# Optimization experiments

Hardware: AMD Instinct MI355X
Metric: run time of the kernel (lower is better)

Reference implementation:

```python
import jax, jax.numpy as jnp
import numpy as np

B, T, S, D, H = 16, 128, 128, 512, 100

def setup_inputs() -> dict:
    key = jax.random.key(0)
    ks = jax.random.split(key, 10)
    sc = 0.02
    return {
        "input": jax.random.normal(ks[0], (B, T, D), dtype=jnp.float32),
        "memory_bank": jax.random.normal(ks[1], (B, S, D), dtype=jnp.float32),
        "W_in": jax.random.normal(ks[2], (D, D), dtype=jnp.float32) * sc,   # linear_in, no bias
        "W1": jax.random.normal(ks[3], (H, 2 * D), dtype=jnp.float32) * sc,  # linear_1
        "b1": jnp.zeros((H,), dtype=jnp.float32),
        "W2": jax.random.normal(ks[4], (H, H), dtype=jnp.float32) * sc,      # linear_2
        "b2": jnp.zeros((H,), dtype=jnp.float32),
        "w_mean": jax.random.normal(ks[5], (H,), dtype=jnp.float32) * sc,    # mean_out
        "b_mean": jnp.zeros((1,), dtype=jnp.float32),
        "w_var": jax.random.normal(ks[6], (H,), dtype=jnp.float32) * sc,     # var_out
        "b_var": jnp.zeros((1,), dtype=jnp.float32),
        "W_out": jax.random.normal(ks[7], (D, 2 * D), dtype=jnp.float32) * sc,  # linear_out, no bias
    }


def reference(input, memory_bank, W_in, W1, b1, W2, b2, w_mean, b_mean, w_var, b_var, W_out):
    d = input.shape[-1]
    # score(): linear_in(h_t) then bmm with h_s^T -> [B,T,S]
    ht = jnp.einsum('btd,ed->bte', input, W_in)
    align = jnp.einsum('bte,bse->bts', ht, memory_bank)
    # softmax over source dim (no memory_lengths -> no mask)
    align_vectors = jax.nn.softmax(align, axis=-1)
    # get_raw_scores(): fused form of cat([h_t_expand, h_s_expand]) @ W1^T
    W1t, W1s = W1[:, :d], W1[:, d:]
    pt = jnp.einsum('btd,hd->bth', input, W1t)        # [B,T,H]
    ps = jnp.einsum('bsd,hd->bsh', memory_bank, W1s)  # [B,S,H]
    h1 = jax.nn.softplus(pt[:, :, None, :] + ps[:, None, :, :] + b1)  # [B,T,S,H]
    h2 = jax.nn.softplus(jnp.einsum('btsh,gh->btsg', h1, W2) + b2)    # [B,T,S,H]
    h_mean = jax.nn.softplus(jnp.einsum('btsg,g->bts', h2, w_mean) + b_mean[0])
    h_var = jax.nn.softplus(jnp.einsum('btsg,g->bts', h2, w_var) + b_var[0])
    # context + output projection + tanh
    c = jnp.einsum('bts,bsd->btd', align_vectors, memory_bank)
    concat_c = jnp.concatenate([c, input], axis=-1)  # [B,T,2D]
    attn_h = jnp.tanh(jnp.einsum('btf,df->btd', concat_c, W_out))
    # multi-step: transpose to [T,B,*]
    attn_h = jnp.transpose(attn_h, (1, 0, 2))
    align_vectors = jnp.transpose(align_vectors, (1, 0, 2))
    return attn_h, align_vectors, h_mean, h_var
```

## Files before the change

### kernel.cpp

```cpp
#include <hip/hip_runtime.h>
#include <hip/hip_bf16.h>
#include <math.h>

#define Bn 16
#define Tn 128
#define Sn 128
#define Dn 512
#define Hn 100
#define TT 4

typedef short short8 __attribute__((ext_vector_type(8)));
typedef float f32x4 __attribute__((ext_vector_type(4)));
typedef unsigned short ushort4v __attribute__((ext_vector_type(4)));

__device__ __forceinline__ float softplus_f(float x) {
    return fmaxf(x, 0.0f) + __logf(1.0f + __expf(-fabsf(x)));
}
__device__ __forceinline__ unsigned short f2bf(float f) {
    unsigned u = __float_as_uint(f);
    unsigned r = u + 0x7FFFu + ((u >> 16) & 1u);
    return (unsigned short)(r >> 16);
}
__device__ __forceinline__ float bf2f(unsigned short h) {
    return __uint_as_float(((unsigned)h) << 16);
}
__device__ __forceinline__ unsigned pkrn(float a, float b) {
    __hip_bfloat162 h = __float22bfloat162_rn(float2{a, b});
    return *reinterpret_cast<unsigned*>(&h);
}
struct BfPair { unsigned short h, l; };
__device__ __forceinline__ BfPair split2(float x) {
    BfPair p;
    p.h = f2bf(x);
    p.l = f2bf(x - bf2f(p.h));
    return p;
}

__global__ __launch_bounds__(256)
void conv_trans(const float* __restrict__ input, const float* __restrict__ mem,
                const float* __restrict__ W_in, const float* __restrict__ W1,
                const float* __restrict__ W_out, const float* __restrict__ W2,
                unsigned short* __restrict__ inh, unsigned short* __restrict__ inl,
                unsigned short* __restrict__ memh, unsigned short* __restrict__ meml,
                unsigned short* __restrict__ winh, unsigned short* __restrict__ winl,
                unsigned short* __restrict__ w1b, unsigned short* __restrict__ woutb,
                unsigned short* __restrict__ w2b, unsigned short* __restrict__ concatb,
                unsigned short* __restrict__ memTb)
{
    __shared__ float tile[64][65];
    const int bx = blockIdx.x;
    if (bx >= 2930) {
        const int b2x = bx - 2930;
        const int d0 = (b2x & 7) * 64, s0 = ((b2x >> 3) & 1) * 64, b = b2x >> 4;
        const int tid = threadIdx.x;
        const int r = tid >> 2, cb = (tid & 3) * 16;
        const float* src = mem + ((long)b * Sn + s0 + r) * Dn + d0 + cb;
        #pragma unroll
        for (int j = 0; j < 4; ++j) {
            float4 v = *(const float4*)&src[j * 4];
            tile[r][cb + j * 4 + 0] = v.x;
            tile[r][cb + j * 4 + 1] = v.y;
            tile[r][cb + j * 4 + 2] = v.z;
            tile[r][cb + j * 4 + 3] = v.w;
        }
        __syncthreads();
        unsigned short* dst = memTb + ((long)b * Dn + d0 + r) * Sn + s0 + cb;
        #pragma unroll
        for (int j = 0; j < 4; ++j) {
            ushort4v q;
            q.x = f2bf(tile[cb + j * 4 + 0][r]);
            q.y = f2bf(tile[cb + j * 4 + 1][r]);
            q.z = f2bf(tile[cb + j * 4 + 2][r]);
            q.w = f2bf(tile[cb + j * 4 + 3][r]);
            *(ushort4v*)&dst[j * 4] = q;
        }
        return;
    }
    long gid = (long)bx * 1024 + (long)threadIdx.x * 4;
    if (gid < 1048576) {
        float4 v = *(const float4*)&input[gid];
        BfPair a = split2(v.x), b = split2(v.y), c = split2(v.z), d = split2(v.w);
        ushort4v h = {a.h, b.h, c.h, d.h};
        ushort4v l = {a.l, b.l, c.l, d.l};
        *(ushort4v*)&inh[gid] = h;
        *(ushort4v*)&inl[gid] = l;
        long row = gid >> 9; int col = (int)(gid & 511);
        *(ushort4v*)&concatb[row * 1024 + 512 + col] = h;
    } else if (gid < 2097152) {
        long e = gid - 1048576;
        float4 v = *(const float4*)&mem[e];
        BfPair a = split2(v.x), b = split2(v.y), c = split2(v.z), d = split2(v.w);
        ushort4v h = {a.h, b.h, c.h, d.h};
        ushort4v l = {a.l, b.l, c.l, d.l};
        *(ushort4v*)&memh[e] = h;
        *(ushort4v*)&meml[e] = l;
    } else if (gid < 2359296) {
        long e = gid - 2097152;
        float4 v = *(const float4*)&W_in[e];
        BfPair a = split2(v.x), b = split2(v.y), c = split2(v.z), d = split2(v.w);
        ushort4v h = {a.h, b.h, c.h, d.h};
        ushort4v l = {a.l, b.l, c.l, d.l};
        *(ushort4v*)&winh[e] = h;
        *(ushort4v*)&winl[e] = l;
    } else if (gid < 2461696) {
        long e = gid - 2359296;
        float4 v = *(const float4*)&W1[e];
        ushort4v h = {f2bf(v.x), f2bf(v.y), f2bf(v.z), f2bf(v.w)};
        *(ushort4v*)&w1b[e] = h;
    } else if (gid < 2985984) {
        long e = gid - 2461696;
        float4 v = *(const float4*)&W_out[e];
        ushort4v h = {f2bf(v.x), f2bf(v.y), f2bf(v.z), f2bf(v.w)};
        *(ushort4v*)&woutb[e] = h;
    } else {
        long e = gid - 2985984;
        int n = (int)(e >> 7), k = (int)(e & 127);
        ushort4v h;
        #pragma unroll
        for (int j = 0; j < 4; ++j) {
            int kj = k + j;
            float val = (n < Hn && kj < Hn) ? W2[n * Hn + kj] : 0.0f;
            h[j] = f2bf(val);
        }
        *(ushort4v*)&w2b[n * 128 + k] = h;
    }
}

template<int SPLIT, int EPI, int KSPLIT, int BSEL>
__device__ __forceinline__
void gemm_body(int bx, int by, int bz_in, int upperThresh,
               const unsigned short* __restrict__ Ah, const unsigned short* __restrict__ Al,
               const unsigned short* __restrict__ Bh, const unsigned short* __restrict__ Bl,
               float* __restrict__ C, unsigned short* __restrict__ Cb,
               unsigned short* __restrict__ Cb2, const float* __restrict__ bias,
               int N, int K, int lda, int ldb, int ldc,
               long sA, long sB, long sC, long sKC,
               unsigned short* As_, unsigned short* Bs_)
{
    unsigned short* Asl = As_ + 4096;
    unsigned short* Bsl = Bs_ + 4096;

    const int tid = threadIdx.x;
    const int n0 = bx * 64;
    const long m0 = (long)by * 64;
    int bz = bz_in, kh = 0;
    if (KSPLIT) { bz = bz_in & 15; kh = bz_in >> 4; }
    Ah += (long)bz * sA;
    Bh += (long)bz * sB;
    if (SPLIT) { Al += (long)bz * sA; Bl += (long)bz * sB; }
    const bool upperB = BSEL && (by >= upperThresh);
    if (upperB) Bh += BSEL;

    const int kbeg = KSPLIT ? kh * (K / KSPLIT) : 0;
    const int kend = KSPLIT ? kbeg + (K / KSPLIT) : K;

    const int wid = tid >> 6, lane = tid & 63;
    const int lm = lane & 15, lq = lane >> 4;
    const int wm = wid & 1, wn = wid >> 1;

    const int sr = tid >> 2;
    const int sc = (tid & 3) * 2;
    const bool bok = (n0 + sr) < N;

    f32x4 acc[2][2];
    #pragma unroll
    for (int i = 0; i < 2; ++i)
        #pragma unroll
        for (int j = 0; j < 2; ++j)
            acc[i][j] = (f32x4){0.f, 0.f, 0.f, 0.f};

    for (int k0 = kbeg; k0 < kend; k0 += 64) {
        __syncthreads();
        #pragma unroll
        for (int i = 0; i < 2; ++i) {
            int c = sc + i, p = c ^ (sr & 7);
            *(short8*)&As_[sr * 64 + p * 8] =
                *(const short8*)&Ah[(m0 + sr) * lda + k0 + c * 8];
            if (SPLIT)
                *(short8*)&Asl[sr * 64 + p * 8] =
                    *(const short8*)&Al[(m0 + sr) * lda + k0 + c * 8];
        }
        #pragma unroll
        for (int i = 0; i < 2; ++i) {
            int c = sc + i, p = c ^ (sr & 7);
            short8 v = {0, 0, 0, 0, 0, 0, 0, 0};
            short8 vl = {0, 0, 0, 0, 0, 0, 0, 0};
            if (bok) {
                v = *(const short8*)&Bh[(long)(n0 + sr) * ldb + k0 + c * 8];
                if (SPLIT) vl = *(const short8*)&Bl[(long)(n0 + sr) * ldb + k0 + c * 8];
            }
            *(short8*)&Bs_[sr * 64 + p * 8] = v;
            if (SPLIT) *(short8*)&Bsl[sr * 64 + p * 8] = vl;
        }
        __syncthreads();
        #pragma unroll
        for (int kst = 0; kst < 2; ++kst) {
            short8 a[2], b[2], a2[2], b2r[2];
            const int pp = (kst * 4 + lq) ^ (lm & 7);
            #pragma unroll
            for (int mt = 0; mt < 2; ++mt) {
                int row = wm * 32 + mt * 16 + lm;
                a[mt] = *(const short8*)&As_[row * 64 + pp * 8];
                if (SPLIT) a2[mt] = *(const short8*)&Asl[row * 64 + pp * 8];
            }
            #pragma unroll
            for (int nt = 0; nt < 2; ++nt) {
                int row = wn * 32 + nt * 16 + lm;
                b[nt] = *(const short8*)&Bs_[row * 64 + pp * 8];
                if (SPLIT) b2r[nt] = *(const short8*)&Bsl[row * 64 + pp * 8];
            }
            #pragma unroll
            for (int mt = 0; mt < 2; ++mt)
                #pragma unroll
                for (int nt = 0; nt < 2; ++nt) {
                    if (SPLIT) {
                        acc[mt][nt] = __builtin_amdgcn_mfma_f32_16x16x32_bf16(
                            a2[mt], b[nt], acc[mt][nt], 0, 0, 0);
                        acc[mt][nt] = __builtin_amdgcn_mfma_f32_16x16x32_bf16(
                            a[mt], b2r[nt], acc[mt][nt], 0, 0, 0);
                    }
                    acc[mt][nt] = __builtin_amdgcn_mfma_f32_16x16x32_bf16(
                        a[mt], b[nt], acc[mt][nt], 0, 0, 0);
                }
        }
    }

    #pragma unroll
    for (int mt = 0; mt < 2; ++mt)
        #pragma unroll
        for (int nt = 0; nt < 2; ++nt)
            #pragma unroll
            for (int r = 0; r < 4; ++r) {
                long m = m0 + wm * 32 + mt * 16 + lq * 4 + r;
                int n = n0 + wn * 32 + nt * 16 + lm;
                float v = acc[mt][nt][r];
                if (EPI == 0) {
                    if (n < N)
                        C[(long)bz * sC + (long)kh * sKC + m * ldc + n] = v;
                } else if (EPI == 1) {
                    unsigned short h = f2bf(v);
                    Cb[m * ldc + n] = h;
                    Cb2[m * ldc + n] = f2bf(v - bf2f(h));
                } else if (EPI == 2) {
                    long bb = m >> 7, tt = m & 127;
                    C[tt * (Bn * Dn) + bb * Dn + n] = tanhf(v);
                } else if (EPI == 3) {
                    Cb[(long)bz * sC + m * ldc + n] = f2bf(v);
                } else {
                    float bb = (!upperB && n < Hn) ? bias[n] : 0.f;
                    C[m * ldc + n] = v + bb;
                }
            }
}

template<int SPLIT, int EPI, int KSPLIT, int BSEL>
__global__ __launch_bounds__(256)
void mfma_gemm3(const unsigned short* __restrict__ Ah, const unsigned short* __restrict__ Al,
                const unsigned short* __restrict__ Bh, const unsigned short* __restrict__ Bl,
                float* __restrict__ C, unsigned short* __restrict__ Cb,
                unsigned short* __restrict__ Cb2, const float* __restrict__ bias,
                int N, int K, int lda, int ldb, int ldc,
                long sA, long sB, long sC, long sKC)
{
    __shared__ __align__(16) unsigned short As_[(SPLIT ? 2 : 1) * 4096];
    __shared__ __align__(16) unsigned short Bs_[(SPLIT ? 2 : 1) * 4096];
    gemm_body<SPLIT, EPI, KSPLIT, BSEL>(blockIdx.x, blockIdx.y, blockIdx.z,
        (int)(gridDim.y >> 1), Ah, Al, Bh, Bl, C, Cb, Cb2, bias,
        N, K, lda, ldb, ldc, sA, sB, sC, sKC, As_, Bs_);
}

__global__ __launch_bounds__(256)
void gemm_ht_ptps(const unsigned short* __restrict__ inh, const unsigned short* __restrict__ inl,
                  const unsigned short* __restrict__ winh, const unsigned short* __restrict__ winl,
                  unsigned short* __restrict__ hth, unsigned short* __restrict__ htl,
                  const unsigned short* __restrict__ w1b, float* __restrict__ ptps,
                  const float* __restrict__ b1)
{
    __shared__ __align__(16) unsigned short As_[8192];
    __shared__ __align__(16) unsigned short Bs_[8192];
    const int id = blockIdx.x;
    if (id < 256) {
        gemm_body<1, 1, 0, 0>(id & 7, id >> 3, 0, 0,
            inh, inl, winh, winl, nullptr, hth, htl, nullptr,
            Dn, Dn, Dn, Dn, Dn, 0L, 0L, 0L, 0L, As_, Bs_);
    } else {
        const int j = id - 256;
        gemm_body<0, 4, 0, 512>(j & 1, j >> 1, 0, 32,
            inh, nullptr, w1b, nullptr, ptps, nullptr, nullptr, b1,
            Hn, Dn, Dn, 2 * Dn, 128, 0L, 0L, 0L, 0L, As_, Bs_);
    }
}

__global__ __launch_bounds__(256)
void mlp_mfma5(const float* __restrict__ ptps,
               const unsigned short* __restrict__ w2b,
               const float* __restrict__ b2,
               const float* __restrict__ w_mean, const float* __restrict__ b_mean,
               const float* __restrict__ w_var, const float* __restrict__ b_var,
               float* __restrict__ mean_out, float* __restrict__ var_out)
{
    __shared__ __align__(16) unsigned short w2s[112 * 128];
    __shared__ float ptl[TT][132];
    __shared__ float wpk[224];
    __shared__ float b2l[112];

    const int tg = blockIdx.x;
    const int b  = blockIdx.y & 15;
    const int s0 = (blockIdx.y >> 4) * 64;
    const int tid = threadIdx.x;

    #pragma unroll
    for (int i0 = 0; i0 < 7; ++i0) {
        int i = tid + i0 * 256;
        int r_ = i >> 4, c_ = i & 15;
        *(short8*)&w2s[r_ * 128 + (c_ ^ (r_ & 7)) * 8] = *(const short8*)&w2b[i * 8];
    }
    #pragma unroll
    for (int j = 0; j < 2; ++j) {
        int i = tid + j * 256;
        int tt = i >> 7, c = i & 127;
        ptl[tt][c] = ptps[((long)b * Tn + tg * TT + tt) * 128 + c];
    }
    if (tid < 224) {
        int g = tid >> 1;
        wpk[tid] = (g < Hn) ? ((tid & 1) ? w_var[g] : w_mean[g]) : 0.f;
    }
    if (tid < 112) b2l[tid] = (tid < Hn) ? b2[tid] : 0.f;

    const int wid = tid >> 6, lane = tid & 63;
    const int lm = lane & 15, lq = lane >> 4;
    const int s = s0 + wid * 16 + lm;

    float psreg[4][8];
    {
        const float* psrow = ptps + (long)(2048 + b * Sn + s) * 128;
        #pragma unroll
        for (int ks = 0; ks < 4; ++ks) {
            *(float4*)&psreg[ks][0] = *(const float4*)&psrow[ks * 32 + lq * 8];
            *(float4*)&psreg[ks][4] = *(const float4*)&psrow[ks * 32 + lq * 8 + 4];
        }
    }
    const float bm = b_mean[0], bv = b_var[0];
    __syncthreads();

    for (int t = 0; t < TT; ++t) {
        f32x4 acc[7];
        #pragma unroll
        for (int j = 0; j < 7; ++j) acc[j] = (f32x4){0.f, 0.f, 0.f, 0.f};

        #pragma unroll
        for (int ks = 0; ks < 4; ++ks) {
            float4 pa = *(const float4*)&ptl[t][ks * 32 + lq * 8];
            float4 pb = *(const float4*)&ptl[t][ks * 32 + lq * 8 + 4];
            float x0 = softplus_f(psreg[ks][0] + pa.x);
            float x1 = softplus_f(psreg[ks][1] + pa.y);
            float x2 = softplus_f(psreg[ks][2] + pa.z);
            float x3 = softplus_f(psreg[ks][3] + pa.w);
            float x4 = softplus_f(psreg[ks][4] + pb.x);
            float x5 = softplus_f(psreg[ks][5] + pb.y);
            float x6 = softplus_f(psreg[ks][6] + pb.z);
            float x7 = softplus_f(psreg[ks][7] + pb.w);
            union { uint4 u4; short8 s8; } cv;
            cv.u4.x = pkrn(x0, x1); cv.u4.y = pkrn(x2, x3);
            cv.u4.z = pkrn(x4, x5); cv.u4.w = pkrn(x6, x7);
            const short8 hf = cv.s8;
            const int p = (ks * 4 + lq) ^ (lm & 7);
            #pragma unroll
            for (int mt = 0; mt < 7; ++mt) {
                short8 w = *(const short8*)&w2s[(mt * 16 + lm) * 128 + p * 8];
                acc[mt] = __builtin_amdgcn_mfma_f32_16x16x32_bf16(w, hf, acc[mt], 0, 0, 0);
            }
        }
        float sM = 0.f, sV = 0.f;
        #pragma unroll
        for (int mt = 0; mt < 7; ++mt) {
            const int g0 = mt * 16 + lq * 4;
            float4 bg = *(const float4*)&b2l[g0];
            float4 wa = *(const float4*)&wpk[g0 * 2];
            float4 wb = *(const float4*)&wpk[g0 * 2 + 4];
            float h2;
            h2 = softplus_f(acc[mt][0] + bg.x); sM = fmaf(h2, wa.x, sM); sV = fmaf(h2, wa.y, sV);
            h2 = softplus_f(acc[mt][1] + bg.y); sM = fmaf(h2, wa.z, sM); sV = fmaf(h2, wa.w, sV);
            h2 = softplus_f(acc[mt][2] + bg.z); sM = fmaf(h2, wb.x, sM); sV = fmaf(h2, wb.y, sV);
            h2 = softplus_f(acc[mt][3] + bg.w); sM = fmaf(h2, wb.z, sM); sV = fmaf(h2, wb.w, sV);
        }
        sM += __shfl_xor(sM, 16); sM += __shfl_xor(sM, 32);
        sV += __shfl_xor(sV, 16); sV += __shfl_xor(sV, 32);
        if (lq == 0) {
            const long base = ((long)b * Tn + tg * TT + t) * Sn + s;
            mean_out[base] = softplus_f(sM + bm);
            var_out[base]  = softplus_f(sV + bv);
        }
    }
}

__global__ __launch_bounds__(256)
void softmax_c(const float* __restrict__ algn, long kstride,
               const unsigned short* __restrict__ memTb,
               float* __restrict__ av_out, unsigned short* __restrict__ concatb)
{
    __shared__ __align__(16) unsigned short avs[64 * 128];
    __shared__ __align__(16) unsigned short Bs[64 * 128];

    const int ntb = blockIdx.x, mtb = blockIdx.y, b = blockIdx.z;
    const int tid = threadIdx.x;
    const int r = tid >> 2, q = tid & 3;

    float v[32];
    {
        const float* arow = algn + ((long)b * Tn + mtb * 64 + r) * Sn + q * 32;
        #pragma unroll
        for (int j = 0; j < 8; ++j) {
            float4 a0 = *(const float4*)&arow[j * 4];
            float4 a1 = *(const float4*)&arow[j * 4 + kstride];
            float4 a2 = *(const float4*)&arow[j * 4 + 2 * kstride];
            float4 a3 = *(const float4*)&arow[j * 4 + 3 * kstride];
            v[j * 4 + 0] = a0.x + a1.x + a2.x + a3.x;
            v[j * 4 + 1] = a0.y + a1.y + a2.y + a3.y;
            v[j * 4 + 2] = a0.z + a1.z + a2.z + a3.z;
            v[j * 4 + 3] = a0.w + a1.w + a2.w + a3.w;
        }
    }
    float mx = v[0];
    #pragma unroll
    for (int i = 1; i < 32; ++i) mx = fmaxf(mx, v[i]);
    mx = fmaxf(mx, __shfl_xor(mx, 1));
    mx = fmaxf(mx, __shfl_xor(mx, 2));
    float sum = 0.f;
    #pragma unroll
    for (int i = 0; i < 32; ++i) { v[i] = __expf(v[i] - mx); sum += v[i]; }
    sum += __shfl_xor(sum, 1);
    sum += __shfl_xor(sum, 2);
    const float inv = 1.0f / sum;

    if (ntb == 0) {
        float* dst = av_out + (long)(mtb * 64 + r) * (Bn * Sn) + b * Sn + q * 32;
        #pragma unroll
        for (int j = 0; j < 8; ++j) {
            float4 o = {v[j*4]*inv, v[j*4+1]*inv, v[j*4+2]*inv, v[j*4+3]*inv};
            *(float4*)&dst[j * 4] = o;
        }
    }
    #pragma unroll
    for (int i = 0; i < 4; ++i) {
        int c = q * 4 + i;
        uint4 u;
        u.x = pkrn(v[i*8+0]*inv, v[i*8+1]*inv);
        u.y = pkrn(v[i*8+2]*inv, v[i*8+3]*inv);
        u.z = pkrn(v[i*8+4]*inv, v[i*8+5]*inv);
        u.w = pkrn(v[i*8+6]*inv, v[i*8+7]*inv);
        *(uint4*)&avs[r * 128 + (c ^ (r & 7)) * 8] = u;
    }
    #pragma unroll
    for (int j = 0; j < 4; ++j) {
        int idx = tid * 4 + j;
        int rB = idx >> 4, cB = idx & 15;
        *(short8*)&Bs[rB * 128 + (cB ^ (rB & 7)) * 8] =
            *(const short8*)&memTb[((long)b * Dn + ntb * 64 + rB) * Sn + cB * 8];
    }
    __syncthreads();

    const int wid = tid >> 6, lane = tid & 63;
    const int lm = lane & 15, lq = lane >> 4;
    const int wm = wid & 1, wn = wid >> 1;

    f32x4 acc[2][2];
    #pragma unroll
    for (int i = 0; i < 2; ++i)
        #pragma unroll
        for (int j = 0; j < 2; ++j) acc[i][j] = (f32x4){0.f, 0.f, 0.f, 0.f};

    #pragma unroll
    for (int kk = 0; kk < 4; ++kk) {
        const int p = (kk * 4 + lq) ^ (lm & 7);
        short8 a0 = *(const short8*)&avs[(wm * 32 + lm) * 128 + p * 8];
        short8 a1 = *(const short8*)&avs[(wm * 32 + 16 + lm) * 128 + p * 8];
        short8 b0 = *(const short8*)&Bs[(wn * 32 + lm) * 128 + p * 8];
        short8 b1 = *(const short8*)&Bs[(wn * 32 + 16 + lm) * 128 + p * 8];
        acc[0][0] = __builtin_amdgcn_mfma_f32_16x16x32_bf16(a0, b0, acc[0][0], 0, 0, 0);
        acc[0][1] = __builtin_amdgcn_mfma_f32_16x16x32_bf16(a0, b1, acc[0][1], 0, 0, 0);
        acc[1][0] = __builtin_amdgcn_mfma_f32_16x16x32_bf16(a1, b0, acc[1][0], 0, 0, 0);
        acc[1][1] = __builtin_amdgcn_mfma_f32_16x16x32_bf16(a1, b1, acc[1][1], 0, 0, 0);
    }
    #pragma unroll
    for (int mt = 0; mt < 2; ++mt)
        #pragma unroll
        for (int nt = 0; nt < 2; ++nt)
            #pragma unroll
            for (int rr = 0; rr < 4; ++rr) {
                long mrow = (long)b * Tn + mtb * 64 + wm * 32 + mt * 16 + lq * 4 + rr;
                int n = ntb * 64 + wn * 32 + nt * 16 + lm;
                concatb[mrow * 1024 + n] = f2bf(acc[mt][nt][rr]);
            }
}

extern "C" void kernel_launch(void* const* d_in, const int* in_sizes, int n_in,
                              void* d_out, int out_size, void* d_ws, size_t ws_size,
                              hipStream_t stream)
{
    (void)in_sizes; (void)n_in; (void)out_size; (void)ws_size;

    const float* input  = (const float*)d_in[0];
    const float* mem    = (const float*)d_in[1];
    const float* W_in   = (const float*)d_in[2];
    const float* W1     = (const float*)d_in[3];
    const float* b1     = (const float*)d_in[4];
    const float* W2     = (const float*)d_in[5];
    const float* b2     = (const float*)d_in[6];
    const float* w_mean = (const float*)d_in[7];
    const float* b_mean = (const float*)d_in[8];
    const float* w_var  = (const float*)d_in[9];
    const float* b_var  = (const float*)d_in[10];
    const float* W_out  = (const float*)d_in[11];

    float* out      = (float*)d_out;
    float* attn_out = out;
    float* av_out   = out + (long)Tn * Bn * Dn;
    float* mean_out = av_out + (long)Tn * Bn * Sn;
    float* var_out  = mean_out + (long)Bn * Tn * Sn;

    char* p = (char*)d_ws;
    unsigned short* inh   = (unsigned short*)p; p += 2097152;
    unsigned short* memh  = (unsigned short*)p; p += 2097152;
    unsigned short* inl   = (unsigned short*)p; p += 2097152;
    unsigned short* meml  = (unsigned short*)p; p += 2097152;
    unsigned short* winh  = (unsigned short*)p; p += 524288;
    unsigned short* winl  = (unsigned short*)p; p += 524288;
    unsigned short* w1b   = (unsigned short*)p; p += 204800;
    unsigned short* woutb = (unsigned short*)p; p += 1048576;
    unsigned short* w2b   = (unsigned short*)p; p += 28672;
    unsigned short* memTb = (unsigned short*)p; p += 2097152;
    unsigned short* hth   = (unsigned short*)p; p += 2097152;
    unsigned short* htl   = (unsigned short*)p; p += 2097152;
    float* ptps           = (float*)p;          p += 2097152;
    float* algn           = (float*)p;          p += 4194304;
    unsigned short* concatb = (unsigned short*)p; p += 4194304;

    const long kstride = (long)Bn * Tn * Sn;

    conv_trans<<<dim3(2930 + 256), 256, 0, stream>>>(
        input, mem, W_in, W1, W_out, W2,
        inh, inl, memh, meml, winh, winl, w1b, woutb, w2b, concatb, memTb);

    gemm_ht_ptps<<<dim3(384), 256, 0, stream>>>(
        inh, inl, winh, winl, hth, htl, w1b, ptps, b1);

    mfma_gemm3<1, 0, 4, 0><<<dim3(2, 2, 64), 256, 0, stream>>>(
        hth, htl, memh, meml, algn, nullptr, nullptr, nullptr,
        Sn, Dn, Dn, Dn, Sn, (long)Tn * Dn, (long)Sn * Dn,
        (long)Tn * Sn, kstride);

    mlp_mfma5<<<dim3(32, 32), 256, 0, stream>>>(
        ptps, w2b, b2, w_mean, b_mean, w_var, b_var, mean_out, var_out);

    softmax_c<<<dim3(8, 2, 16), 256, 0, stream>>>(
        algn, kstride, memTb, av_out, concatb);

    mfma_gemm3<0, 2, 0, 0><<<dim3(8, 32), 256, 0, stream>>>(
        concatb, nullptr, woutb, nullptr, attn_out, nullptr, nullptr, nullptr,
        Dn, 2 * Dn, 2 * Dn, 2 * Dn, Dn, 0L, 0L, 0L, 0L);
}
```

Measured before the change: 191.4 us.

## Prefetch GEMM tiles into registers and restructure MLP kernel via shared h1 tile

The generic GEMM body now loads the next K-tile from global memory into registers while MFMAs run on the current shared-memory tile, so global latency overlaps compute. Separately, the MLP kernel is replaced by an older-style variant: it computes h1 cooperatively into a shared-memory tile, runs MFMAs with h1 as the A operand and W2 as B, and reduces mean/var with a 16-lane shuffle tree. Each block now covers 2 time steps instead of 4, so the grid doubles and W2 is staged into shared memory twice as often. This also adds extra barriers per step and raises register pressure in the GEMM.

```diff
diff --git a/kernel.cpp b/kernel.cpp
--- a/kernel.cpp
+++ b/kernel.cpp
@@ -7,7 +7,7 @@
 #define Sn 128
 #define Dn 512
 #define Hn 100
-#define TT 4
+#define TT2 2
 
 typedef short short8 __attribute__((ext_vector_type(8)));
 typedef float f32x4 __attribute__((ext_vector_type(4)));
@@ -169,30 +169,42 @@
         for (int j = 0; j < 2; ++j)
             acc[i][j] = (f32x4){0.f, 0.f, 0.f, 0.f};
 
+    short8 pA[2], pB[2], pAl[2], pBl[2];
+    const short8 zz = {0, 0, 0, 0, 0, 0, 0, 0};
+
+    #pragma unroll
+    for (int i = 0; i < 2; ++i) {
+        int c = sc + i;
+        pA[i] = *(const short8*)&Ah[(m0 + sr) * lda + kbeg + c * 8];
+        if (SPLIT) pAl[i] = *(const short8*)&Al[(m0 + sr) * lda + kbeg + c * 8];
+        pB[i] = bok ? *(const short8*)&Bh[(long)(n0 + sr) * ldb + kbeg + c * 8] : zz;
+        if (SPLIT) pBl[i] = bok ? *(const short8*)&Bl[(long)(n0 + sr) * ldb + kbeg + c * 8] : zz;
+    }
+
     for (int k0 = kbeg; k0 < kend; k0 += 64) {
         __syncthreads();
         #pragma unroll
         for (int i = 0; i < 2; ++i) {
             int c = sc + i, p = c ^ (sr & 7);
-            *(short8*)&As_[sr * 64 + p * 8] =
-                *(const short8*)&Ah[(m0 + sr) * lda + k0 + c * 8];
-            if (SPLIT)
-                *(short8*)&Asl[sr * 64 + p * 8] =
-                    *(const short8*)&Al[(m0 + sr) * lda + k0 + c * 8];
-        }
-        #pragma unroll
-        for (int i = 0; i < 2; ++i) {
-            int c = sc + i, p = c ^ (sr & 7);
-            short8 v = {0, 0, 0, 0, 0, 0, 0, 0};
-            short8 vl = {0, 0, 0, 0, 0, 0, 0, 0};
-            if (bok) {
-                v = *(const short8*)&Bh[(long)(n0 + sr) * ldb + k0 + c * 8];
-                if (SPLIT) vl = *(const short8*)&Bl[(long)(n0 + sr) * ldb + k0 + c * 8];
-            }
-            *(short8*)&Bs_[sr * 64 + p * 8] = v;
-            if (SPLIT) *(short8*)&Bsl[sr * 64 + p * 8] = vl;
+            *(short8*)&As_[sr * 64 + p * 8] = pA[i];
+            *(short8*)&Bs_[sr * 64 + p * 8] = pB[i];
+            if (SPLIT) {
+                *(short8*)&Asl[sr * 64 + p * 8] = pAl[i];
+                *(short8*)&Bsl[sr * 64 + p * 8] = pBl[i];
+            }
         }
         __syncthreads();
+        if (k0 + 64 < kend) {
+            const int kn = k0 + 64;
+            #pragma unroll
+            for (int i = 0; i < 2; ++i) {
+                int c = sc + i;
+                pA[i] = *(const short8*)&Ah[(m0 + sr) * lda + kn + c * 8];
+                if (SPLIT) pAl[i] = *(const short8*)&Al[(m0 + sr) * lda + kn + c * 8];
+                pB[i] = bok ? *(const short8*)&Bh[(long)(n0 + sr) * ldb + kn + c * 8] : zz;
+                if (SPLIT) pBl[i] = bok ? *(const short8*)&Bl[(long)(n0 + sr) * ldb + kn + c * 8] : zz;
+            }
+        }
         #pragma unroll
         for (int kst = 0; kst < 2; ++kst) {
             short8 a[2], b[2], a2[2], b2r[2];
@@ -292,21 +304,21 @@
 }
 
 __global__ __launch_bounds__(256)
-void mlp_mfma5(const float* __restrict__ ptps,
+void mlp_mfma4(const float* __restrict__ ptps,
                const unsigned short* __restrict__ w2b,
                const float* __restrict__ b2,
                const float* __restrict__ w_mean, const float* __restrict__ b_mean,
                const float* __restrict__ w_var, const float* __restrict__ b_var,
                float* __restrict__ mean_out, float* __restrict__ var_out)
 {
+    __shared__ __align__(16) unsigned short h1s[64 * 128];
     __shared__ __align__(16) unsigned short w2s[112 * 128];
-    __shared__ float ptl[TT][132];
-    __shared__ float wpk[224];
-    __shared__ float b2l[112];
+    __shared__ float ptl[TT2][140];
+    __shared__ float b2p[112], wmp[112], wvp[112];
 
     const int tg = blockIdx.x;
-    const int b  = blockIdx.y & 15;
-    const int s0 = (blockIdx.y >> 4) * 64;
+    const int b  = blockIdx.y >> 1;
+    const int s0 = (blockIdx.y & 1) * 64;
     const int tid = threadIdx.x;
 
     #pragma unroll
@@ -315,82 +327,100 @@
         int r_ = i >> 4, c_ = i & 15;
         *(short8*)&w2s[r_ * 128 + (c_ ^ (r_ & 7)) * 8] = *(const short8*)&w2b[i * 8];
     }
-    #pragma unroll
-    for (int j = 0; j < 2; ++j) {
-        int i = tid + j * 256;
-        int tt = i >> 7, c = i & 127;
-        ptl[tt][c] = ptps[((long)b * Tn + tg * TT + tt) * 128 + c];
-    }
-    if (tid < 224) {
-        int g = tid >> 1;
-        wpk[tid] = (g < Hn) ? ((tid & 1) ? w_var[g] : w_mean[g]) : 0.f;
-    }
-    if (tid < 112) b2l[tid] = (tid < Hn) ? b2[tid] : 0.f;
+    {
+        int t = tid >> 7, c = tid & 127;
+        ptl[t][c + 4 * (c >> 5)] =
+            ptps[((long)b * Tn + tg * TT2 + t) * 128 + c];
+    }
+    if (tid < 112) {
+        b2p[tid] = (tid < Hn) ? b2[tid] : 0.f;
+        wmp[tid] = (tid < Hn) ? w_mean[tid] : 0.f;
+        wvp[tid] = (tid < Hn) ? w_var[tid] : 0.f;
+    }
+
+    const int r = tid >> 2, cb = tid & 3;
+    float psreg[4][8];
+    {
+        const float* psrow = ptps + (long)(2048 + b * Sn + s0 + r) * 128;
+        #pragma unroll
+        for (int i = 0; i < 4; ++i) {
+            int col = (cb + 4 * i) * 8;
+            *(float4*)&psreg[i][0] = *(const float4*)&psrow[col];
+            *(float4*)&psreg[i][4] = *(const float4*)&psrow[col + 4];
+        }
+    }
+    __syncthreads();
 
     const int wid = tid >> 6, lane = tid & 63;
     const int lm = lane & 15, lq = lane >> 4;
-    const int s = s0 + wid * 16 + lm;
-
-    float psreg[4][8];
-    {
-        const float* psrow = ptps + (long)(2048 + b * Sn + s) * 128;
+    const float bm = b_mean[0], bv = b_var[0];
+
+    for (int t = 0; t < TT2; ++t) {
+        #pragma unroll
+        for (int i = 0; i < 4; ++i) {
+            const int c = cb + 4 * i;
+            const int col = c * 8;
+            const int base = col + 4 * (col >> 5);
+            float4 pa = *(const float4*)&ptl[t][base];
+            float4 pb = *(const float4*)&ptl[t][base + 4];
+            float x0 = softplus_f(psreg[i][0] + pa.x);
+            float x1 = softplus_f(psreg[i][1] + pa.y);
+            float x2 = softplus_f(psreg[i][2] + pa.z);
+            float x3 = softplus_f(psreg[i][3] + pa.w);
+            float x4 = softplus_f(psreg[i][4] + pb.x);
+            float x5 = softplus_f(psreg[i][5] + pb.y);
+            float x6 = softplus_f(psreg[i][6] + pb.z);
+            float x7 = softplus_f(psreg[i][7] + pb.w);
+            uint4 u;
+            u.x = pkrn(x0, x1); u.y = pkrn(x2, x3);
+            u.z = pkrn(x4, x5); u.w = pkrn(x6, x7);
+            *(uint4*)&h1s[r * 128 + (c ^ (r & 7)) * 8] = u;
+        }
+        __syncthreads();
+
+        f32x4 acc[7];
+        #pragma unroll
+        for (int j = 0; j < 7; ++j) acc[j] = (f32x4){0.f, 0.f, 0.f, 0.f};
         #pragma unroll
         for (int ks = 0; ks < 4; ++ks) {
-            *(float4*)&psreg[ks][0] = *(const float4*)&psrow[ks * 32 + lq * 8];
-            *(float4*)&psreg[ks][4] = *(const float4*)&psrow[ks * 32 + lq * 8 + 4];
-        }
-    }
-    const float bm = b_mean[0], bv = b_var[0];
-    __syncthreads();
-
-    for (int t = 0; t < TT; ++t) {
-        f32x4 acc[7];
-        #pragma unroll
-        for (int j = 0; j < 7; ++j) acc[j] = (f32x4){0.f, 0.f, 0.f, 0.f};
-
-        #pragma unroll
-        for (int ks = 0; ks < 4; ++ks) {
-            float4 pa = *(const float4*)&ptl[t][ks * 32 + lq * 8];
-            float4 pb = *(const float4*)&ptl[t][ks * 32 + lq * 8 + 4];
-            float x0 = softplus_f(psreg[ks][0] + pa.x);
-            float x1 = softplus_f(psreg[ks][1] + pa.y);
-            float x2 = softplus_f(psreg[ks][2] + pa.z);
-            float x3 = softplus_f(psreg[ks][3] + pa.w);
-            float x4 = softplus_f(psreg[ks][4] + pb.x);
-            float x5 = softplus_f(psreg[ks][5] + pb.y);
-            float x6 = softplus_f(psreg[ks][6] + pb.z);
-            float x7 = softplus_f(psreg[ks][7] + pb.w);
-            union { uint4 u4; short8 s8; } cv;
-            cv.u4.x = pkrn(x0, x1); cv.u4.y = pkrn(x2, x3);
-            cv.u4.z = pkrn(x4, x5); cv.u4.w = pkrn(x6, x7);
-            const short8 hf = cv.s8;
             const int p = (ks * 4 + lq) ^ (lm & 7);
-            #pragma unroll
-            for (int mt = 0; mt < 7; ++mt) {
-                short8 w = *(const short8*)&w2s[(mt * 16 + lm) * 128 + p * 8];
-                acc[mt] = __builtin_amdgcn_mfma_f32_16x16x32_bf16(w, hf, acc[mt], 0, 0, 0);
-            }
-        }
-        float sM = 0.f, sV = 0.f;
-        #pragma unroll
-        for (int mt = 0; mt < 7; ++mt) {
-            const int g0 = mt * 16 + lq * 4;
-            float4 bg = *(const float4*)&b2l[g0];
-            float4 wa = *(const float4*)&wpk[g0 * 2];
-            float4 wb = *(const float4*)&wpk[g0 * 2 + 4];
-            float h2;
-            h2 = softplus_f(acc[mt][0] + bg.x); sM = fmaf(h2, wa.x, sM); sV = fmaf(h2, wa.y, sV);
-            h2 = softplus_f(acc[mt][1] + bg.y); sM = fmaf(h2, wa.z, sM); sV = fmaf(h2, wa.w, sV);
-            h2 = softplus_f(acc[mt][2] + bg.z); sM = fmaf(h2, wb.x, sM); sV = fmaf(h2, wb.y, sV);
-            h2 = softplus_f(acc[mt][3] + bg.w); sM = fmaf(h2, wb.z, sM); sV = fmaf(h2, wb.w, sV);
-        }
-        sM += __shfl_xor(sM, 16); sM += __shfl_xor(sM, 32);
-        sV += __shfl_xor(sV, 16); sV += __shfl_xor(sV, 32);
-        if (lq == 0) {
-            const long base = ((long)b * Tn + tg * TT + t) * Sn + s;
-            mean_out[base] = softplus_f(sM + bm);
-            var_out[base]  = softplus_f(sV + bv);
-        }
+            short8 a = *(const short8*)&h1s[(wid * 16 + lm) * 128 + p * 8];
+            #pragma unroll
+            for (int nt = 0; nt < 7; ++nt) {
+                short8 bf = *(const short8*)&w2s[(nt * 16 + lm) * 128 + p * 8];
+                acc[nt] = __builtin_amdgcn_mfma_f32_16x16x32_bf16(a, bf, acc[nt], 0, 0, 0);
+            }
+        }
+
+        float sM[4] = {}, sV[4] = {};
+        #pragma unroll
+        for (int nt = 0; nt < 7; ++nt) {
+            int g = nt * 16 + lm;
+            float bg = b2p[g], wm_ = wmp[g], wv_ = wvp[g];
+            #pragma unroll
+            for (int rr = 0; rr < 4; ++rr) {
+                float h2 = softplus_f(acc[nt][rr] + bg);
+                sM[rr] = fmaf(h2, wm_, sM[rr]);
+                sV[rr] = fmaf(h2, wv_, sV[rr]);
+            }
+        }
+        #pragma unroll
+        for (int off = 1; off < 16; off <<= 1)
+            #pragma unroll
+            for (int rr = 0; rr < 4; ++rr) {
+                sM[rr] += __shfl_xor(sM[rr], off);
+                sV[rr] += __shfl_xor(sV[rr], off);
+            }
+        if (lm == 0) {
+            const long base = ((long)b * Tn + tg * TT2 + t) * Sn + s0;
+            #pragma unroll
+            for (int rr = 0; rr < 4; ++rr) {
+                int row = wid * 16 + lq * 4 + rr;
+                mean_out[base + row] = softplus_f(sM[rr] + bm);
+                var_out[base + row]  = softplus_f(sV[rr] + bv);
+            }
+        }
+        __syncthreads();
     }
 }
 
@@ -550,7 +580,7 @@
         Sn, Dn, Dn, Dn, Sn, (long)Tn * Dn, (long)Sn * Dn,
         (long)Tn * Sn, kstride);
 
-    mlp_mfma5<<<dim3(32, 32), 256, 0, stream>>>(
+    mlp_mfma4<<<dim3(Tn / TT2, Bn * 2), 256, 0, stream>>>(
         ptps, w2b, b2, w_mean, b_mean, w_var, b_var, mean_out, var_out);
 
     softmax_c<<<dim3(8, 2, 16), 256, 0, stream>>>(
```

Measured after the change: 172.5 us. -9.9%, faster.
